# Kernel optimization log

Hardware: AMD Instinct MI355X
Metric: run time of the kernel (lower is better)

Reference implementation:

```python
import jax, jax.numpy as jnp
import numpy as np

D = 256          # in_channels == out_channels
H = 4            # num_heads (global branch)
HD = D // H      # head_dim
B = 64           # number of graphs
N = 256          # nodes per graph (max nodes for to_dense_batch)
TOT = B * N      # total nodes
E = TOT * 16     # total edges (avg degree 16)


def _glorot(key, shape):
    fan_in, fan_out = shape[0], shape[1]
    s = jnp.sqrt(6.0 / (fan_in + fan_out))
    return jax.random.uniform(key, shape, jnp.float32, -s, s)


def setup_inputs() -> dict:
    key = jax.random.key(0)
    ks = jax.random.split(key, 20)
    x = jax.random.normal(ks[0], (TOT, D), jnp.float32)
    # intra-graph random edges: local endpoints + graph offset
    local = jax.random.randint(ks[1], (2, E), 0, N)
    gid = jax.random.randint(ks[2], (E,), 0, B)
    edge_index = (local + gid[None, :] * N).astype(jnp.int64)
    batch = (jnp.arange(TOT) // N).astype(jnp.int64)  # sorted, equal-size graphs
    inp = {"x": x, "edge_index": edge_index, "batch": batch}
    # local branch (TransformerConv, heads=1): q/k/v + skip linears [in,out]
    names = ["lq", "lk", "lv", "ls", "gq", "gk", "gv", "go"]
    for i, nm in enumerate(names):
        inp[nm + "_w"] = _glorot(ks[3 + i], (D, D))
        inp[nm + "_b"] = jnp.zeros((D,), jnp.float32)
    inp["w_local"] = jnp.float32(0.5)
    inp["w_global"] = jnp.float32(0.5)
    inp["ln_g"] = jnp.ones((D,), jnp.float32)
    inp["ln_b"] = jnp.zeros((D,), jnp.float32)
    return inp


def _forward(x, edge_index, batch, lq_w, lq_b, lk_w, lk_b, lv_w, lv_b, ls_w, ls_b,
             gq_w, gq_b, gk_w, gk_b, gv_w, gv_b, go_w, go_b,
             w_local, w_global, ln_g, ln_b):
    src, dst = edge_index[0], edge_index[1]
    inv_sqrt_d = 1.0 / jnp.sqrt(jnp.float32(D))

    # ---- local branch: TransformerConv (heads=1, root_weight=True) ----
    q = x @ lq_w + lq_b
    k = x @ lk_w + lk_b
    v = x @ lv_w + lv_b
    logits = jnp.sum(q[dst] * k[src], axis=-1) * inv_sqrt_d          # [E]
    m = jax.ops.segment_max(logits, dst, num_segments=TOT)           # per-target max
    ex = jnp.exp(logits - m[dst])
    den = jax.ops.segment_sum(ex, dst, num_segments=TOT)
    alpha = ex / (den[dst] + 1e-16)
    agg = jax.ops.segment_sum(alpha[:, None] * v[src], dst, num_segments=TOT)
    local_out = agg + x @ ls_w + ls_b                                # skip (root) term

    # ---- global branch: to_dense_batch + masked multihead attention ----
    counts = jax.ops.segment_sum(jnp.ones((TOT,), jnp.float32), batch, num_segments=B)
    starts = (jnp.cumsum(counts) - counts).astype(jnp.int32)
    pos = jnp.arange(TOT, dtype=jnp.int32) - starts[batch]
    dense = jnp.zeros((B, N, D), x.dtype).at[batch, pos].set(x)
    mask = jnp.zeros((B, N), bool).at[batch, pos].set(True)

    qh = (dense @ gq_w + gq_b).reshape(B, N, H, HD)
    kh = (dense @ gk_w + gk_b).reshape(B, N, H, HD)
    vh = (dense @ gv_w + gv_b).reshape(B, N, H, HD)
    scores = jnp.einsum('bnhd,bmhd->bhnm', qh, kh) / jnp.sqrt(jnp.float32(HD))
    scores = jnp.where(mask[:, None, None, :], scores, -jnp.inf)     # mask keys
    attn = jax.nn.softmax(scores, axis=-1)
    od = jnp.einsum('bhnm,bmhd->bnhd', attn, vh).reshape(B, N, D)
    od = od @ go_w + go_b
    global_out = od[batch, pos] + x                                  # in==out residual

    # ---- weighted fusion + residual + LayerNorm ----
    fused = w_local * local_out + w_global * global_out
    out = fused + x
    mu = jnp.mean(out, axis=-1, keepdims=True)
    var = jnp.mean(jnp.square(out - mu), axis=-1, keepdims=True)
    out = (out - mu) / jnp.sqrt(var + 1e-5) * ln_g + ln_b
    return out


def reference(x, edge_index, batch, lq_w, lq_b, lk_w, lk_b, lv_w, lv_b, ls_w, ls_b,
              gq_w, gq_b, gk_w, gk_b, gv_w, gv_b, go_w, go_b,
              w_local, w_global, ln_g, ln_b):
    return _forward(x, edge_index, batch, lq_w, lq_b, lk_w, lk_b, lv_w, lv_b,
                    ls_w, ls_b, gq_w, gq_b, gk_w, gk_b, gv_w, gv_b, go_w, go_b,
                    w_local, w_global, ln_g, ln_b)
```

## Files before the change

### kernel.cpp

```cpp
#include <hip/hip_runtime.h>
#include <hip/hip_bf16.h>

#define D_DIM 256
#define NPG   256
#define HEADS 4
#define HD    64
#define BCAP  64

typedef __bf16 bf16x8 __attribute__((ext_vector_type(8)));
typedef __bf16 bf16x4 __attribute__((ext_vector_type(4)));
typedef float  f32x4  __attribute__((ext_vector_type(4)));

__device__ inline float us2f(unsigned short u) {
    union { unsigned int i; float f; } cv; cv.i = ((unsigned int)u) << 16; return cv.f;
}

#define GLOAD_LDS16(g, l) __builtin_amdgcn_global_load_lds(                    \
    (const __attribute__((address_space(1))) void*)(g),                        \
    (__attribute__((address_space(3))) void*)(l), 16, 0, 0)

__global__ __launch_bounds__(256) void prep_misc(const float* __restrict__ x,
                                                 __bf16* __restrict__ xpk,
        const float* w0, const float* w1, const float* w2, const float* w3,
        const float* w4, const float* w5, const float* w6, const float* w7,
        __bf16* __restrict__ wt, int* __restrict__ zeros, int nb1, int tot) {
    __shared__ __bf16 tile[256][16];
    int bid = blockIdx.x;
    const int t = threadIdx.x;
    if (bid < nb1) {
        const int rt = bid;
        const int ks = t >> 5;
        #pragma unroll
        for (int h2 = 0; h2 < 2; ++h2) {
            int lane = (t & 31) * 2 + h2;
            int row = rt * 16 + (lane & 15);
            int col = ks * 32 + (lane >> 4) * 8;
            const float4* src = reinterpret_cast<const float4*>(x + (size_t)row * 256 + col);
            float4 f0 = src[0], f1 = src[1];
            __bf16* o = xpk + ((size_t)(rt * 8 + ks) * 64 + lane) * 8;
            o[0] = (__bf16)f0.x; o[1] = (__bf16)f0.y; o[2] = (__bf16)f0.z; o[3] = (__bf16)f0.w;
            o[4] = (__bf16)f1.x; o[5] = (__bf16)f1.y; o[6] = (__bf16)f1.z; o[7] = (__bf16)f1.w;
        }
        return;
    }
    bid -= nb1;
    if (bid < 128) {
        const float* Ws[8] = {w0, w1, w2, w3, w4, w5, w6, w7};
        const int jt2 = bid & 15, wsel = bid >> 4;
        const float* W = Ws[wsel];
        const float4* wr = reinterpret_cast<const float4*>(W + (size_t)t * 256 + jt2 * 16);
        #pragma unroll
        for (int u = 0; u < 4; ++u) {
            float4 f = wr[u];
            tile[t][u * 4 + 0] = (__bf16)f.x; tile[t][u * 4 + 1] = (__bf16)f.y;
            tile[t][u * 4 + 2] = (__bf16)f.z; tile[t][u * 4 + 3] = (__bf16)f.w;
        }
        __syncthreads();
        __bf16* out = wt + ((size_t)wsel * 16 + jt2) * 4096;
        #pragma unroll
        for (int u = 0; u < 16; ++u) {
            int e = t * 16 + u;
            int ks = e >> 9, lane = (e >> 3) & 63, i = e & 7;
            int g = lane >> 4, c = lane & 15;
            int k = ks * 32 + g * 8 + i;
            out[e] = tile[k][c];
        }
        return;
    }
    bid -= 128;
    int i = bid * 256 + t;
    if (i < tot) zeros[i] = 0;
}

__global__ __launch_bounds__(512) void proj_csr(const __bf16* __restrict__ xpk,
                                                const __bf16* __restrict__ wt,
        const float* b_gq, const float* b_gk, const float* b_gv,
        const float* b_lq, const float* b_lk, const float* b_lv, const float* b_ls,
        __bf16* o_gq, __bf16* o_gk, __bf16* Vt,
        __bf16* o_lq, __bf16* o_lk, __bf16* o_lv, __bf16* o_ls,
        const int* __restrict__ ei_raw, int* __restrict__ bucket,
        int* __restrict__ deg, int E, int nb_gemm, int M) {
    __shared__ __align__(16) __bf16 wlds[16384];
    int bid = blockIdx.x;
    if (bid >= nb_gemm) {
        int v = ei_raw[2 * (threadIdx.x & 63) + 1];
        unsigned long long nz = __ballot(v != 0);
        bool is64 = (nz == 0ULL);
        int e = (bid - nb_gemm) * 512 + threadIdx.x;
        if (e >= E) return;
        int s, d;
        if (is64) { s = ei_raw[2 * e]; d = ei_raw[2 * (E + e)]; }
        else      { s = ei_raw[e];     d = ei_raw[E + e]; }
        int p = atomicAdd(&deg[d], 1);
        if (p < BCAP) bucket[d * BCAP + p] = s;
        return;
    }
    const int gx = M >> 8;
    const int cpx = gx >> 3;
    const int xcd = bid & 7;
    const int local = bid >> 3;
    const int x = xcd * cpx + (local % cpx);
    const int y = local / cpx;
    const int j = y >> 2;
    const int q = y & 3;
    const int wsel = (j < 3) ? j : j + 1;
    const float* bias = (j == 0) ? b_gq : (j == 1) ? b_gk : (j == 2) ? b_gv :
                        (j == 3) ? b_lq : (j == 4) ? b_lk : (j == 5) ? b_lv : b_ls;
    __bf16* C = (j == 0) ? o_gq : (j == 1) ? o_gk : (j == 2) ? nullptr :
                (j == 3) ? o_lq : (j == 4) ? o_lk : (j == 5) ? o_lv : o_ls;

    {
        const __bf16* gs = wt + (size_t)wsel * 65536 + (size_t)q * 16384;
        #pragma unroll
        for (int it = 0; it < 4; ++it) {
            int ch = it * 512 + threadIdx.x;
            GLOAD_LDS16(gs + ch * 8, wlds + ch * 8);
        }
    }

    const int wid = threadIdx.x >> 6, lane = threadIdx.x & 63;
    const int g = lane >> 4, c = lane & 15;
    const int rt0 = x * 16 + wid * 2;
    const char* wl = reinterpret_cast<const char*>(wlds) + lane * 16;

    __syncthreads();

    f32x4 acc[2][4];
    #pragma unroll
    for (int h = 0; h < 2; ++h)
        #pragma unroll
        for (int jt = 0; jt < 4; ++jt) acc[h][jt] = (f32x4){0.f, 0.f, 0.f, 0.f};

    const __bf16* ap0 = xpk + ((size_t)rt0 * 8) * 512 + lane * 8;
    const __bf16* ap1 = ap0 + 8 * 512;
    #pragma unroll
    for (int ks = 0; ks < 8; ++ks) {
        bf16x8 af0 = *reinterpret_cast<const bf16x8*>(ap0 + ks * 512);
        bf16x8 af1 = *reinterpret_cast<const bf16x8*>(ap1 + ks * 512);
        #pragma unroll
        for (int jt = 0; jt < 4; ++jt) {
            bf16x8 bf_ = *reinterpret_cast<const bf16x8*>(wl + (jt * 8 + ks) * 1024);
            acc[0][jt] = __builtin_amdgcn_mfma_f32_16x16x32_bf16(bf_, af0, acc[0][jt], 0, 0, 0);
            acc[1][jt] = __builtin_amdgcn_mfma_f32_16x16x32_bf16(bf_, af1, acc[1][jt], 0, 0, 0);
        }
    }

    if (j == 2) {
        #pragma unroll
        for (int h = 0; h < 2; ++h) {
            int m = (rt0 + h) * 16 + c;
            int b = m >> 8, mm = m & 255;
            #pragma unroll
            for (int jt = 0; jt < 4; ++jt) {
                int col0 = q * 64 + jt * 16 + g * 4;
                float4 bv = *reinterpret_cast<const float4*>(bias + col0);
                Vt[(size_t)(b * 256 + col0 + 0) * 256 + mm] = (__bf16)(acc[h][jt][0] + bv.x);
                Vt[(size_t)(b * 256 + col0 + 1) * 256 + mm] = (__bf16)(acc[h][jt][1] + bv.y);
                Vt[(size_t)(b * 256 + col0 + 2) * 256 + mm] = (__bf16)(acc[h][jt][2] + bv.z);
                Vt[(size_t)(b * 256 + col0 + 3) * 256 + mm] = (__bf16)(acc[h][jt][3] + bv.w);
            }
        }
    } else {
        __syncthreads();
        char* ob = reinterpret_cast<char*>(wlds);
        #pragma unroll
        for (int h = 0; h < 2; ++h) {
            int row_local = wid * 32 + h * 16 + c;
            int swz = (row_local & 7) << 4;
            #pragma unroll
            for (int jt = 0; jt < 4; ++jt) {
                int col2 = jt * 16 + g * 4;
                float4 bv = *reinterpret_cast<const float4*>(bias + q * 64 + col2);
                bf16x4 st;
                st[0] = (__bf16)(acc[h][jt][0] + bv.x);
                st[1] = (__bf16)(acc[h][jt][1] + bv.y);
                st[2] = (__bf16)(acc[h][jt][2] + bv.z);
                st[3] = (__bf16)(acc[h][jt][3] + bv.w);
                int bo = (row_local * 128 + col2 * 2) ^ swz;
                *reinterpret_cast<bf16x4*>(ob + bo) = st;
            }
        }
        __syncthreads();
        #pragma unroll
        for (int i = 0; i < 4; ++i) {
            int rl = wid * 32 + i * 8 + (lane >> 3);
            int bo = (rl * 128 + (lane & 7) * 16) ^ ((rl & 7) << 4);
            bf16x8 vd = *reinterpret_cast<const bf16x8*>(ob + bo);
            *reinterpret_cast<bf16x8*>(
                &C[(size_t)(x * 256 + rl) * 256 + q * 64 + (lane & 7) * 8]) = vd;
        }
    }
}

__global__ __launch_bounds__(256) void global_attn_mfma(const __bf16* __restrict__ Qb,
                                                        const __bf16* __restrict__ Kb,
                                                        const __bf16* __restrict__ Vt,
                                                        __bf16* __restrict__ od) {
    __shared__ __align__(16) char lds[65536];
    const int tid = threadIdx.x;
    const int wid = tid >> 6, lane = tid & 63;
    const int bh = blockIdx.x >> 2, qq = blockIdx.x & 3;
    const int b = bh >> 2, h = bh & 3;
    const int qb = qq * 4 + wid;
    const int g = lane >> 4, c = lane & 15;

    {
        const __bf16* kgp = Kb + ((size_t)b * 256) * 256 + h * 64;
        int krow = tid >> 3, ch = tid & 7;
        #pragma unroll
        for (int p = 0; p < 8; ++p) {
            int kk = p * 32 + krow;
            bf16x8 val = *reinterpret_cast<const bf16x8*>(kgp + (size_t)kk * 256 + ch * 8);
            int bo = (kk * 128 + ch * 16) ^ ((kk & 7) << 4);
            *reinterpret_cast<bf16x8*>(lds + bo) = val;
        }
    }
    {
        const bf16x8* vgp = reinterpret_cast<const bf16x8*>(Vt + (size_t)bh * 16384);
        #pragma unroll
        for (int p = 0; p < 8; ++p) {
            int off = p * 256 + tid;
            bf16x8 val = vgp[off];
            int row = off >> 5;
            int colb = (off & 31) * 16;
            int bo = 32768 + ((row * 512 + colb) ^ ((row & 7) << 4));
            *reinterpret_cast<bf16x8*>(lds + bo) = val;
        }
    }
    const __bf16* qptr = Qb + ((size_t)(b * 256 + qb * 16 + c)) * 256 + h * 64 + g * 8;
    bf16x8 aq0 = *reinterpret_cast<const bf16x8*>(qptr);
    bf16x8 aq1 = *reinterpret_cast<const bf16x8*>(qptr + 32);
    __syncthreads();

    f32x4 S[16];
    #pragma unroll
    for (int jt = 0; jt < 16; ++jt) S[jt] = (f32x4){0.f, 0.f, 0.f, 0.f};
    #pragma unroll
    for (int jt = 0; jt < 16; ++jt) {
        int key = jt * 16 + c;
        int sw = (key & 7) << 4;
        int bo0 = (key * 128 + g * 16) ^ sw;
        int bo1 = (key * 128 + 64 + g * 16) ^ sw;
        bf16x8 bk0 = *reinterpret_cast<const bf16x8*>(lds + bo0);
        bf16x8 bk1 = *reinterpret_cast<const bf16x8*>(lds + bo1);
        S[jt] = __builtin_amdgcn_mfma_f32_16x16x32_bf16(aq0, bk0, S[jt], 0, 0, 0);
        S[jt] = __builtin_amdgcn_mfma_f32_16x16x32_bf16(aq1, bk1, S[jt], 0, 0, 0);
    }

    float rmax[4] = {-3e38f, -3e38f, -3e38f, -3e38f};
    #pragma unroll
    for (int jt = 0; jt < 16; ++jt)
        #pragma unroll
        for (int r = 0; r < 4; ++r) {
            float s = S[jt][r] * 0.125f;
            S[jt][r] = s;
            rmax[r] = fmaxf(rmax[r], s);
        }
    #pragma unroll
    for (int r = 0; r < 4; ++r) {
        rmax[r] = fmaxf(rmax[r], __shfl_xor(rmax[r], 1));
        rmax[r] = fmaxf(rmax[r], __shfl_xor(rmax[r], 2));
        rmax[r] = fmaxf(rmax[r], __shfl_xor(rmax[r], 4));
        rmax[r] = fmaxf(rmax[r], __shfl_xor(rmax[r], 8));
    }
    float rsum[4] = {0.f, 0.f, 0.f, 0.f};
    #pragma unroll
    for (int jt = 0; jt < 16; ++jt)
        #pragma unroll
        for (int r = 0; r < 4; ++r) {
            float e = __expf(S[jt][r] - rmax[r]);
            S[jt][r] = e;
            rsum[r] += e;
        }
    #pragma unroll
    for (int r = 0; r < 4; ++r) {
        rsum[r] += __shfl_xor(rsum[r], 1);
        rsum[r] += __shfl_xor(rsum[r], 2);
        rsum[r] += __shfl_xor(rsum[r], 4);
        rsum[r] += __shfl_xor(rsum[r], 8);
    }

    __syncthreads();
    char* Pw = lds + wid * 8192;
    #pragma unroll
    for (int jt = 0; jt < 16; ++jt)
        #pragma unroll
        for (int r = 0; r < 4; ++r) {
            int row = g * 4 + r;
            int bo = row * 512 + (jt * 16 + c) * 2;
            bo ^= (row & 7) << 4;
            *reinterpret_cast<__bf16*>(Pw + bo) = (__bf16)S[jt][r];
        }
    __syncthreads();

    f32x4 O[4];
    #pragma unroll
    for (int dt = 0; dt < 4; ++dt) O[dt] = (f32x4){0.f, 0.f, 0.f, 0.f};

    #pragma unroll
    for (int mc = 0; mc < 8; ++mc) {
        int bo = c * 512 + (mc * 32 + g * 8) * 2;
        bo ^= (c & 7) << 4;
        bf16x8 ap = *reinterpret_cast<const bf16x8*>(Pw + bo);
        #pragma unroll
        for (int dt = 0; dt < 4; ++dt) {
            int vrow = dt * 16 + c;
            int vbo = 32768 + ((vrow * 512 + mc * 64 + g * 16) ^ ((vrow & 7) << 4));
            bf16x8 bv = *reinterpret_cast<const bf16x8*>(lds + vbo);
            O[dt] = __builtin_amdgcn_mfma_f32_16x16x32_bf16(ap, bv, O[dt], 0, 0, 0);
        }
    }

    #pragma unroll
    for (int dt = 0; dt < 4; ++dt)
        #pragma unroll
        for (int r = 0; r < 4; ++r) {
            int n = b * 256 + qb * 16 + g * 4 + r;
            int col = h * 64 + dt * 16 + c;
            od[(size_t)n * 256 + col] = (__bf16)(O[dt][r] / rsum[r]);
        }
}

__global__ __launch_bounds__(256) void lattn_go(
        const __bf16* __restrict__ ql, const __bf16* __restrict__ kl,
        const __bf16* __restrict__ vl,
        const int* __restrict__ bucket, const int* __restrict__ deg,
        __bf16* __restrict__ aggb,
        const __bf16* __restrict__ od, const __bf16* __restrict__ Wp,
        const float* __restrict__ go_b, __bf16* __restrict__ od2b,
        int nlb, int M, int tot) {
    __shared__ __align__(16) __bf16 wlds[16384];
    int bid = blockIdx.x;
    const int wid = threadIdx.x >> 6, lane = threadIdx.x & 63;
    const int g = lane >> 4, c = lane & 15;

    if (bid >= nlb) {
        int gb = bid - nlb;
        const int gxg = M >> 6;
        const int bx = gb % gxg, by = gb / gxg;
        {
            const __bf16* gs = Wp + (size_t)by * 16384;
            #pragma unroll
            for (int it = 0; it < 8; ++it) {
                int chunk = it * 256 + threadIdx.x;
                GLOAD_LDS16(gs + chunk * 8, wlds + chunk * 8);
            }
        }
        const int row0 = bx * 64 + wid * 16;
        const __bf16* arow = od + (size_t)(row0 + c) * 256 + g * 8;
        bf16x8 af = *reinterpret_cast<const bf16x8*>(arow);

        f32x4 acc[4];
        #pragma unroll
        for (int jt = 0; jt < 4; ++jt) acc[jt] = (f32x4){0.f, 0.f, 0.f, 0.f};

        const char* wl = reinterpret_cast<const char*>(wlds) + lane * 16;
        __syncthreads();
        #pragma unroll
        for (int ks = 0; ks < 8; ++ks) {
            bf16x8 nf;
            if (ks < 7) nf = *reinterpret_cast<const bf16x8*>(arow + (ks + 1) * 32);
            #pragma unroll
            for (int jt = 0; jt < 4; ++jt) {
                bf16x8 bf_ = *reinterpret_cast<const bf16x8*>(wl + (jt * 8 + ks) * 1024);
                acc[jt] = __builtin_amdgcn_mfma_f32_16x16x32_bf16(bf_, af, acc[jt], 0, 0, 0);
            }
            af = nf;
        }
        int row = row0 + c;
        #pragma unroll
        for (int jt = 0; jt < 4; ++jt) {
            int col0 = by * 64 + jt * 16 + g * 4;
            float4 bv = *reinterpret_cast<const float4*>(go_b + col0);
            bf16x4 st;
            st[0] = (__bf16)(acc[jt][0] + bv.x);
            st[1] = (__bf16)(acc[jt][1] + bv.y);
            st[2] = (__bf16)(acc[jt][2] + bv.z);
            st[3] = (__bf16)(acc[jt][3] + bv.w);
            *reinterpret_cast<bf16x4*>(&od2b[(size_t)row * 256 + col0]) = st;
        }
        return;
    }

    int lb = (bid & 7) * (nlb >> 3) + (bid >> 3);
    int w = (lb * 256 + (int)threadIdx.x) >> 6;
    if (w >= tot) return;
    const int t = w;
    const int cc = c;

    float qf[16];
    {
        const ushort4* qr = reinterpret_cast<const ushort4*>(ql + (size_t)t * 256);
        #pragma unroll
        for (int u = 0; u < 4; ++u) {
            ushort4 qv = qr[cc * 4 + u];
            qf[u * 4 + 0] = us2f(qv.x); qf[u * 4 + 1] = us2f(qv.y);
            qf[u * 4 + 2] = us2f(qv.z); qf[u * 4 + 3] = us2f(qv.w);
        }
    }

    int dg = deg[t];
    if (dg > BCAP) dg = BCAP;
    const int* bkt = bucket + (size_t)t * BCAP;
    float M_ = -3.0e38f, den = 0.f;
    float a0 = 0.f, a1 = 0.f, a2 = 0.f, a3 = 0.f;

    for (int i0 = 0; i0 < dg; i0 += 4) {
        bool valid = (i0 + g) < dg;
        int s = valid ? bkt[i0 + g] : 0;

        float p = 0.f;
        const ushort4* kr = reinterpret_cast<const ushort4*>(kl + (size_t)s * 256);
        #pragma unroll
        for (int u = 0; u < 4; ++u) {
            ushort4 kv = kr[cc * 4 + u];
            p += qf[u * 4 + 0] * us2f(kv.x) + qf[u * 4 + 1] * us2f(kv.y)
               + qf[u * 4 + 2] * us2f(kv.z) + qf[u * 4 + 3] * us2f(kv.w);
        }
        p += __shfl_xor(p, 1); p += __shfl_xor(p, 2);
        p += __shfl_xor(p, 4); p += __shfl_xor(p, 8);

        float lg[4]; int sj[4];
        #pragma unroll
        for (int jj = 0; jj < 4; ++jj) {
            float pj = __shfl(p, jj * 16);
            int   ssj = __shfl(s, jj * 16);
            bool vj = (i0 + jj) < dg;
            lg[jj] = vj ? pj * 0.0625f : -3.0e38f;
            sj[jj] = vj ? ssj : 0;
        }

        float nM = fmaxf(fmaxf(fmaxf(lg[0], lg[1]), fmaxf(lg[2], lg[3])), M_);
        float sc = __expf(M_ - nM);
        float ex[4];
        #pragma unroll
        for (int jj = 0; jj < 4; ++jj) ex[jj] = __expf(lg[jj] - nM);

        float s0 = 0.f, s1 = 0.f, s2 = 0.f, s3 = 0.f;
        #pragma unroll
        for (int jj = 0; jj < 4; ++jj) {
            ushort4 vv = reinterpret_cast<const ushort4*>(vl + (size_t)sj[jj] * 256)[lane];
            s0 += ex[jj] * us2f(vv.x); s1 += ex[jj] * us2f(vv.y);
            s2 += ex[jj] * us2f(vv.z); s3 += ex[jj] * us2f(vv.w);
        }
        a0 = a0 * sc + s0; a1 = a1 * sc + s1;
        a2 = a2 * sc + s2; a3 = a3 * sc + s3;
        den = den * sc + ex[0] + ex[1] + ex[2] + ex[3];
        M_ = nM;
    }
    float inv = (dg > 0) ? 1.0f / den : 0.0f;
    bf16x4 o;
    o[0] = (__bf16)(a0 * inv); o[1] = (__bf16)(a1 * inv);
    o[2] = (__bf16)(a2 * inv); o[3] = (__bf16)(a3 * inv);
    reinterpret_cast<bf16x4*>(aggb + (size_t)t * 256)[lane] = o;
}

__global__ __launch_bounds__(256) void fuse_ln(const float* __restrict__ x,
                                               const __bf16* __restrict__ aggb,
                                               const __bf16* __restrict__ skipb,
                                               const __bf16* __restrict__ od2b,
                                               const float* __restrict__ wl_p,
                                               const float* __restrict__ wg_p,
                                               const float* __restrict__ gam,
                                               const float* __restrict__ bet,
                                               float* __restrict__ out, int tot) {
    int w = (blockIdx.x * 256 + threadIdx.x) >> 6;
    int lane = threadIdx.x & 63;
    if (w >= tot) return;
    const float wl = wl_p[0], wg = wg_p[0];
    size_t base = (size_t)w * 256;
    float4 xv = reinterpret_cast<const float4*>(x + base)[lane];
    ushort4 ag = reinterpret_cast<const ushort4*>(aggb + base)[lane];
    ushort4 sk = reinterpret_cast<const ushort4*>(skipb + base)[lane];
    ushort4 o2 = reinterpret_cast<const ushort4*>(od2b + base)[lane];
    float v[4];
    v[0] = wl * (us2f(ag.x) + us2f(sk.x)) + wg * (us2f(o2.x) + xv.x) + xv.x;
    v[1] = wl * (us2f(ag.y) + us2f(sk.y)) + wg * (us2f(o2.y) + xv.y) + xv.y;
    v[2] = wl * (us2f(ag.z) + us2f(sk.z)) + wg * (us2f(o2.z) + xv.z) + xv.z;
    v[3] = wl * (us2f(ag.w) + us2f(sk.w)) + wg * (us2f(o2.w) + xv.w) + xv.w;

    float s = v[0] + v[1] + v[2] + v[3];
    #pragma unroll
    for (int off = 32; off; off >>= 1) s += __shfl_xor(s, off);
    float mu = s * (1.0f / 256.0f);
    float e[4], ss = 0.f;
    #pragma unroll
    for (int j = 0; j < 4; ++j) { e[j] = v[j] - mu; ss += e[j] * e[j]; }
    #pragma unroll
    for (int off = 32; off; off >>= 1) ss += __shfl_xor(ss, off);
    float rstd = rsqrtf(ss * (1.0f / 256.0f) + 1e-5f);
    float4 go;
    int c0 = lane * 4;
    go.x = e[0] * rstd * gam[c0 + 0] + bet[c0 + 0];
    go.y = e[1] * rstd * gam[c0 + 1] + bet[c0 + 1];
    go.z = e[2] * rstd * gam[c0 + 2] + bet[c0 + 2];
    go.w = e[3] * rstd * gam[c0 + 3] + bet[c0 + 3];
    reinterpret_cast<float4*>(out + base)[lane] = go;
}

extern "C" void kernel_launch(void* const* d_in, const int* in_sizes, int n_in,
                              void* d_out, int out_size, void* d_ws, size_t ws_size,
                              hipStream_t stream) {
    const float* x    = (const float*)d_in[0];
    const int*   ei   = (const int*)d_in[1];
    const float* lq_w = (const float*)d_in[3];  const float* lq_b = (const float*)d_in[4];
    const float* lk_w = (const float*)d_in[5];  const float* lk_b = (const float*)d_in[6];
    const float* lv_w = (const float*)d_in[7];  const float* lv_b = (const float*)d_in[8];
    const float* ls_w = (const float*)d_in[9];  const float* ls_b = (const float*)d_in[10];
    const float* gq_w = (const float*)d_in[11]; const float* gq_b = (const float*)d_in[12];
    const float* gk_w = (const float*)d_in[13]; const float* gk_b = (const float*)d_in[14];
    const float* gv_w = (const float*)d_in[15]; const float* gv_b = (const float*)d_in[16];
    const float* go_w = (const float*)d_in[17]; const float* go_b = (const float*)d_in[18];
    const float* wl   = (const float*)d_in[19]; const float* wg   = (const float*)d_in[20];
    const float* ln_g = (const float*)d_in[21]; const float* ln_b = (const float*)d_in[22];

    const int TOT = in_sizes[0] / D_DIM;
    const int E = in_sizes[1] / 2;
    const int B = TOT / NPG;
    const size_t S = (size_t)TOT * D_DIM;

    __bf16* xpk   = (__bf16*)d_ws;
    __bf16* qg    = xpk + S;
    __bf16* kg    = qg + S;
    __bf16* aggb  = kg + S;
    __bf16* ql    = aggb + S;
    __bf16* kl    = ql + S;
    __bf16* vl    = kl + S;
    __bf16* skipb = vl + S;
    __bf16* od2b  = skipb + S;
    __bf16* Vt    = od2b + S;
    __bf16* od    = Vt + S;
    __bf16* wt    = od + S;
    int* bucket = (int*)(wt + 8 * 65536);
    int* deg    = bucket + (size_t)TOT * BCAP;

    const int nb1 = TOT / 16;
    const int nbz = (TOT + 255) / 256;
    prep_misc<<<nb1 + 128 + nbz, 256, 0, stream>>>(x, xpk,
        gq_w, gk_w, gv_w, go_w, lq_w, lk_w, lv_w, ls_w, wt, deg, nb1, TOT);

    const int nb_gemm = (TOT / 256) * 28;
    const int nb_edge = (E + 511) / 512;
    proj_csr<<<nb_gemm + nb_edge, 512, 0, stream>>>(xpk, wt,
        gq_b, gk_b, gv_b, lq_b, lk_b, lv_b, ls_b,
        qg, kg, Vt, ql, kl, vl, skipb,
        ei, bucket, deg, E, nb_gemm, TOT);

    global_attn_mfma<<<B * HEADS * 4, 256, 0, stream>>>(qg, kg, Vt, od);

    __bf16* wt_go = wt + 3 * 65536;
    const int nlb = TOT / 4;
    const int nb_go = (TOT / 64) * 4;
    lattn_go<<<nlb + nb_go, 256, 0, stream>>>(ql, kl, vl, bucket, deg, aggb,
                                              od, wt_go, go_b, od2b,
                                              nlb, TOT, TOT);

    fuse_ln<<<(TOT + 3) / 4, 256, 0, stream>>>(x, aggb, skipb, od2b, wl, wg, ln_g, ln_b,
                                               (float*)d_out, TOT);
}
```

Baseline: 109.8 us.

## Process eight neighbors per step with register-held bucket and prefetched K/V loads

Reworks the local-attention edge loop to handle eight neighbors per iteration instead of four. Eight lanes now cover each key with 16-byte loads. The neighbor index list is loaded once into a register per lane and broadcast with shuffles, and all V rows for the step are issued before any compute. The goal is more memory-level parallelism and fewer dependent global loads per edge. The cost is higher register pressure (32 q floats, 8 V vectors) and wasted work on padded slots when the degree is not a multiple of eight.

Measured after the change: 107.6 us (median of 2 runs). No clear change (-2.0%).

```diff
diff --git a/kernel.cpp b/kernel.cpp
--- a/kernel.cpp
+++ b/kernel.cpp
@@ -13,6 +13,12 @@
 
 __device__ inline float us2f(unsigned short u) {
     union { unsigned int i; float f; } cv; cv.i = ((unsigned int)u) << 16; return cv.f;
+}
+__device__ inline float bl(unsigned int w) {
+    union { unsigned int i; float f; } c; c.i = w << 16; return c.f;
+}
+__device__ inline float bh(unsigned int w) {
+    union { unsigned int i; float f; } c; c.i = w & 0xffff0000u; return c.f;
 }
 
 #define GLOAD_LDS16(g, l) __builtin_amdgcn_global_load_lds(                    \
@@ -386,66 +392,82 @@
     int w = (lb * 256 + (int)threadIdx.x) >> 6;
     if (w >= tot) return;
     const int t = w;
-    const int cc = c;
-
-    float qf[16];
-    {
-        const ushort4* qr = reinterpret_cast<const ushort4*>(ql + (size_t)t * 256);
-        #pragma unroll
-        for (int u = 0; u < 4; ++u) {
-            ushort4 qv = qr[cc * 4 + u];
-            qf[u * 4 + 0] = us2f(qv.x); qf[u * 4 + 1] = us2f(qv.y);
-            qf[u * 4 + 2] = us2f(qv.z); qf[u * 4 + 3] = us2f(qv.w);
-        }
-    }
-
+    const int g8 = lane >> 3;
+    const int c8 = lane & 7;
+
+    int bktreg = bucket[(size_t)t * BCAP + lane];
     int dg = deg[t];
     if (dg > BCAP) dg = BCAP;
-    const int* bkt = bucket + (size_t)t * BCAP;
+
+    float qf[32];
+    {
+        const uint4* qr = reinterpret_cast<const uint4*>(ql + (size_t)t * 256) + c8 * 4;
+        #pragma unroll
+        for (int u = 0; u < 4; ++u) {
+            uint4 qv = qr[u];
+            qf[u * 8 + 0] = bl(qv.x); qf[u * 8 + 1] = bh(qv.x);
+            qf[u * 8 + 2] = bl(qv.y); qf[u * 8 + 3] = bh(qv.y);
+            qf[u * 8 + 4] = bl(qv.z); qf[u * 8 + 5] = bh(qv.z);
+            qf[u * 8 + 6] = bl(qv.w); qf[u * 8 + 7] = bh(qv.w);
+        }
+    }
+
     float M_ = -3.0e38f, den = 0.f;
     float a0 = 0.f, a1 = 0.f, a2 = 0.f, a3 = 0.f;
 
-    for (int i0 = 0; i0 < dg; i0 += 4) {
-        bool valid = (i0 + g) < dg;
-        int s = valid ? bkt[i0 + g] : 0;
+    for (int i0 = 0; i0 < dg; i0 += 8) {
+        bool vK = (i0 + g8) < dg;
+        int sK = __shfl(bktreg, i0 + g8);
+        sK = vK ? sK : 0;
+        int sj[8];
+        #pragma unroll
+        for (int jj = 0; jj < 8; ++jj) {
+            int sv = __shfl(bktreg, i0 + jj);
+            sj[jj] = ((i0 + jj) < dg) ? sv : 0;
+        }
+        const uint4* kr = reinterpret_cast<const uint4*>(kl + (size_t)sK * 256) + c8 * 4;
+        uint4 kv[4];
+        #pragma unroll
+        for (int u = 0; u < 4; ++u) kv[u] = kr[u];
+        ushort4 vv[8];
+        #pragma unroll
+        for (int jj = 0; jj < 8; ++jj)
+            vv[jj] = reinterpret_cast<const ushort4*>(vl + (size_t)sj[jj] * 256)[lane];
 
         float p = 0.f;
-        const ushort4* kr = reinterpret_cast<const ushort4*>(kl + (size_t)s * 256);
         #pragma unroll
         for (int u = 0; u < 4; ++u) {
-            ushort4 kv = kr[cc * 4 + u];
-            p += qf[u * 4 + 0] * us2f(kv.x) + qf[u * 4 + 1] * us2f(kv.y)
-               + qf[u * 4 + 2] * us2f(kv.z) + qf[u * 4 + 3] * us2f(kv.w);
-        }
-        p += __shfl_xor(p, 1); p += __shfl_xor(p, 2);
-        p += __shfl_xor(p, 4); p += __shfl_xor(p, 8);
-
-        float lg[4]; int sj[4];
-        #pragma unroll
-        for (int jj = 0; jj < 4; ++jj) {
-            float pj = __shfl(p, jj * 16);
-            int   ssj = __shfl(s, jj * 16);
-            bool vj = (i0 + jj) < dg;
-            lg[jj] = vj ? pj * 0.0625f : -3.0e38f;
-            sj[jj] = vj ? ssj : 0;
-        }
-
-        float nM = fmaxf(fmaxf(fmaxf(lg[0], lg[1]), fmaxf(lg[2], lg[3])), M_);
+            p += qf[u * 8 + 0] * bl(kv[u].x) + qf[u * 8 + 1] * bh(kv[u].x)
+               + qf[u * 8 + 2] * bl(kv[u].y) + qf[u * 8 + 3] * bh(kv[u].y)
+               + qf[u * 8 + 4] * bl(kv[u].z) + qf[u * 8 + 5] * bh(kv[u].z)
+               + qf[u * 8 + 6] * bl(kv[u].w) + qf[u * 8 + 7] * bh(kv[u].w);
+        }
+        p += __shfl_xor(p, 1); p += __shfl_xor(p, 2); p += __shfl_xor(p, 4);
+
+        float lg[8];
+        #pragma unroll
+        for (int jj = 0; jj < 8; ++jj) {
+            float pj = __shfl(p, jj * 8);
+            lg[jj] = ((i0 + jj) < dg) ? pj * 0.0625f : -3.0e38f;
+        }
+        float nM = M_;
+        #pragma unroll
+        for (int jj = 0; jj < 8; ++jj) nM = fmaxf(nM, lg[jj]);
         float sc = __expf(M_ - nM);
-        float ex[4];
-        #pragma unroll
-        for (int jj = 0; jj < 4; ++jj) ex[jj] = __expf(lg[jj] - nM);
+        float ex[8];
+        float esum = 0.f;
+        #pragma unroll
+        for (int jj = 0; jj < 8; ++jj) { ex[jj] = __expf(lg[jj] - nM); esum += ex[jj]; }
 
         float s0 = 0.f, s1 = 0.f, s2 = 0.f, s3 = 0.f;
         #pragma unroll
-        for (int jj = 0; jj < 4; ++jj) {
-            ushort4 vv = reinterpret_cast<const ushort4*>(vl + (size_t)sj[jj] * 256)[lane];
-            s0 += ex[jj] * us2f(vv.x); s1 += ex[jj] * us2f(vv.y);
-            s2 += ex[jj] * us2f(vv.z); s3 += ex[jj] * us2f(vv.w);
+        for (int jj = 0; jj < 8; ++jj) {
+            s0 += ex[jj] * us2f(vv[jj].x); s1 += ex[jj] * us2f(vv[jj].y);
+            s2 += ex[jj] * us2f(vv[jj].z); s3 += ex[jj] * us2f(vv[jj].w);
         }
         a0 = a0 * sc + s0; a1 = a1 * sc + s1;
         a2 = a2 * sc + s2; a3 = a3 * sc + s3;
-        den = den * sc + ex[0] + ex[1] + ex[2] + ex[3];
+        den = den * sc + esum;
         M_ = nM;
     }
     float inv = (dg > 0) ? 1.0f / den : 0.0f;
```
